# Performance work log

Hardware: AMD Instinct MI355X
Metric: run time of the kernel (lower is better)

## Reference

```python
import jax, jax.numpy as jnp
import numpy as np

N_EMBD = 1024
N_HEAD = 16
HEAD = N_EMBD // N_HEAD


def setup_inputs() -> dict:
    key = jax.random.key(0)
    ks = jax.random.split(key, 5)
    B, T = 2, 2048
    s = 1.0 / np.sqrt(N_EMBD)
    return {
        "x": jax.random.normal(ks[0], (B, T, N_EMBD), dtype=jnp.float32),
        "w_attn": jax.random.normal(ks[1], (N_EMBD, 3 * N_EMBD), dtype=jnp.float32) * s,
        "b_attn": jnp.zeros((3 * N_EMBD,), dtype=jnp.float32),
        "w_proj": jax.random.normal(ks[2], (N_EMBD, N_EMBD), dtype=jnp.float32) * s,
        "b_proj": jnp.zeros((N_EMBD,), dtype=jnp.float32),
    }


def reference(x, w_attn, b_attn, w_proj, b_proj):
    B, T, C = x.shape
    qkv = x @ w_attn + b_attn                      # [B,T,3C]
    q, k, v = jnp.split(qkv, 3, axis=-1)
    def heads(t):
        return t.reshape(B, T, N_HEAD, HEAD).transpose(0, 2, 1, 3)  # [B,H,T,D]
    q, k, v = heads(q), heads(k), heads(v)
    scale = 1.0 / np.sqrt(HEAD).astype(np.float32)
    scores = jnp.einsum('bhqd,bhkd->bhqk', q, k) * scale
    causal = jnp.tril(jnp.ones((T, T), dtype=bool))
    scores = jnp.where(causal, scores, -jnp.inf)
    attn = jax.nn.softmax(scores, axis=-1)
    out = jnp.einsum('bhqk,bhkd->bhqd', attn, v)   # [B,H,T,D]
    out = out.transpose(0, 2, 1, 3).reshape(B, T, C)
    return out @ w_proj + b_proj
```

## Files before the change

kernel.cpp:

```cpp
#include <hip/hip_runtime.h>
#include <stdint.h>

#define N_EMBD 1024
#define N_HEADv 16
#define HEADv 64
#define Bv 2
#define Tv 2048
#define BT (Bv*Tv)
#define C3 (3*N_EMBD)

typedef __attribute__((ext_vector_type(8))) short bf16x8;
typedef __attribute__((ext_vector_type(4))) float f32x4;

typedef __attribute__((address_space(3))) uint32_t lds_u32;
typedef const __attribute__((address_space(1))) uint32_t glb_u32;

__device__ __forceinline__ void gload_lds16(const void* g, void* l){
  __builtin_amdgcn_global_load_lds((glb_u32*)g, (lds_u32*)l, 16, 0, 0);
}

__device__ __forceinline__ unsigned short f2bf(float f){
  union { float f; uint32_t u; } v; v.f = f;
  uint32_t u = v.u;
  uint32_t r = u + 0x7FFFu + ((u>>16)&1u);
  return (unsigned short)(r>>16);
}
__device__ __forceinline__ float bf2f(unsigned short s){
  union { uint32_t u; float f; } v; v.u = ((uint32_t)s)<<16; return v.f;
}
__device__ __forceinline__ uint32_t cvt_pk_bf16(float lo, float hi){
  uint32_t r;
  asm("v_cvt_pk_bf16_f32 %0, %1, %2" : "=v"(r) : "v"(lo), "v"(hi));
  return r;
}

__global__ __launch_bounds__(256) void k_prep(
    const float* __restrict__ x, unsigned short* __restrict__ xb,
    const float* __restrict__ w_attn, unsigned short* __restrict__ wat,
    const float* __restrict__ w_proj, unsigned short* __restrict__ wpt)
{
  __shared__ float tile[64][65];
  int blk = blockIdx.x;
  int t = threadIdx.x;
  if(blk < 2048){
    long i = ((long)blk*256 + t)*8;
    float4 a = *reinterpret_cast<const float4*>(x+i);
    float4 b = *reinterpret_cast<const float4*>(x+i+4);
    union { int4 v; unsigned short s[8]; } o;
    o.s[0]=f2bf(a.x); o.s[1]=f2bf(a.y); o.s[2]=f2bf(a.z); o.s[3]=f2bf(a.w);
    o.s[4]=f2bf(b.x); o.s[5]=f2bf(b.y); o.s[6]=f2bf(b.z); o.s[7]=f2bf(b.w);
    *reinterpret_cast<int4*>(xb+i) = o.v;
  } else {
    const float* in; unsigned short* out; int K, N, n0, k0;
    if(blk < 2816){
      int b = blk - 2048;
      in = w_attn; out = wat; K = N_EMBD; N = C3;
      n0 = (b % 48)*64; k0 = (b / 48)*64;
    } else {
      int b = blk - 2816;
      in = w_proj; out = wpt; K = N_EMBD; N = N_EMBD;
      n0 = (b % 16)*64; k0 = (b / 16)*64;
    }
    #pragma unroll
    for(int p=0;p<4;p++){
      int row = (t>>4) + p*16;
      int col4 = (t&15)*4;
      float4 v = *reinterpret_cast<const float4*>(&in[(size_t)(k0+row)*N + n0 + col4]);
      tile[row][col4+0]=v.x; tile[row][col4+1]=v.y; tile[row][col4+2]=v.z; tile[row][col4+3]=v.w;
    }
    __syncthreads();
    #pragma unroll
    for(int p=0;p<4;p++){
      int nrow = (t>>4) + p*16;
      int kc = (t&15)*4;
      ushort4 o;
      o.x = f2bf(tile[kc+0][nrow]);
      o.y = f2bf(tile[kc+1][nrow]);
      o.z = f2bf(tile[kc+2][nrow]);
      o.w = f2bf(tile[kc+3][nrow]);
      *reinterpret_cast<ushort4*>(&out[(size_t)(n0+nrow)*K + k0 + kc]) = o;
    }
  }
}

template<int MODE, int FM, int FN>
__global__ __launch_bounds__(256) void k_gemm(
    const unsigned short* __restrict__ A,
    const unsigned short* __restrict__ Bt,
    const float* __restrict__ bias,
    void* __restrict__ Cout,
    int M, int N, int K)
{
  const int BK=64;
  const int TM=FM*32, TN=FN*32;
  const int ASZ=TM*BK, BSZ=TN*BK;
  __shared__ unsigned short As[2*ASZ];
  __shared__ unsigned short Bs[2*BSZ];
  int m0 = blockIdx.y*TM, n0 = blockIdx.x*TN;
  int t = threadIdx.x, lane = t&63, wid = t>>6;
  int wm = (wid>>1)*FM*16, wn = (wid&1)*FN*16;
  int g = lane>>4, r16 = lane&15;
  int rl  = lane>>3;
  int cle = (((lane&7) ^ rl) * 8);
  int rsw = r16 & 7;
  f32x4 acc[FM][FN] = {};

  #pragma unroll
  for(int c=0;c<FM;c++){
    int rb = wid*FM*8 + c*8;
    gload_lds16(&A [(size_t)(m0+rb+rl)*K + cle], &As[rb*BK]);
  }
  #pragma unroll
  for(int c=0;c<FN;c++){
    int rb = wid*FN*8 + c*8;
    gload_lds16(&Bt[(size_t)(n0+rb+rl)*K + cle], &Bs[rb*BK]);
  }
  __syncthreads();

  const int NIT = K/BK;
  for(int it=0; it<NIT; ++it){
    int cur = it & 1;
    if(it+1 < NIT){
      int k0 = (it+1)*BK;
      #pragma unroll
      for(int c=0;c<FM;c++){
        int rb = wid*FM*8 + c*8;
        gload_lds16(&A [(size_t)(m0+rb+rl)*K + k0 + cle], &As[(cur^1)*ASZ + rb*BK]);
      }
      #pragma unroll
      for(int c=0;c<FN;c++){
        int rb = wid*FN*8 + c*8;
        gload_lds16(&Bt[(size_t)(n0+rb+rl)*K + k0 + cle], &Bs[(cur^1)*BSZ + rb*BK]);
      }
    }
    const unsigned short* Ab = &As[cur*ASZ];
    const unsigned short* Bb = &Bs[cur*BSZ];
    bf16x8 af[2][FM], bfr[2][FN];
    #pragma unroll
    for(int ks=0;ks<2;ks++){
      #pragma unroll
      for(int mi=0;mi<FM;mi++)
        af[ks][mi]  = *reinterpret_cast<const bf16x8*>(&Ab[(wm+mi*16+r16)*BK + (((ks*4+g)^rsw)*8)]);
      #pragma unroll
      for(int ni=0;ni<FN;ni++)
        bfr[ks][ni] = *reinterpret_cast<const bf16x8*>(&Bb[(wn+ni*16+r16)*BK + (((ks*4+g)^rsw)*8)]);
    }
    __builtin_amdgcn_s_setprio(1);
    #pragma unroll
    for(int ks=0;ks<2;ks++)
      #pragma unroll
      for(int mi=0;mi<FM;mi++)
        #pragma unroll
        for(int ni=0;ni<FN;ni++){
          if(MODE==0)
            acc[mi][ni] = __builtin_amdgcn_mfma_f32_16x16x32_bf16(af[ks][mi], bfr[ks][ni], acc[mi][ni], 0,0,0);
          else
            acc[mi][ni] = __builtin_amdgcn_mfma_f32_16x16x32_bf16(bfr[ks][ni], af[ks][mi], acc[mi][ni], 0,0,0);
        }
    __builtin_amdgcn_s_setprio(0);
    __syncthreads();
  }

  if(MODE==0){
    int which = (n0+wn)>>10;
    int h = ((n0+wn)&1023)>>6;
    int bb = m0>>11;
    int tt0 = (m0&2047) + wm;
    unsigned short* base = (unsigned short*)Cout;
    if(which < 2){
      float scale = (which==0) ? 0.18033688f : 1.0f;
      unsigned short* dst = base + (size_t)which*BT*N_EMBD
                          + (((size_t)bb*N_HEADv + h)*Tv + tt0)*HEADv;
      #pragma unroll
      for(int ni=0;ni<FN;ni++){
        float bv = bias[n0+wn+ni*16+r16];
        int d = ni*16 + r16;
        #pragma unroll
        for(int mi=0;mi<FM;mi++)
          #pragma unroll
          for(int reg=0;reg<4;reg++){
            int tt = mi*16 + g*4 + reg;
            dst[(size_t)tt*HEADv + d] = f2bf((acc[mi][ni][reg] + bv)*scale);
          }
      }
    } else {
      unsigned short* dst = base + 2ll*BT*N_EMBD
                          + (((size_t)bb*N_HEADv + h)*HEADv)*Tv + tt0;
      #pragma unroll
      for(int ni=0;ni<FN;ni++){
        float bv = bias[n0+wn+ni*16+r16];
        int d = ni*16 + r16;
        #pragma unroll
        for(int mi=0;mi<FM;mi++)
          #pragma unroll
          for(int reg=0;reg<4;reg++){
            int tt = mi*16 + g*4 + reg;
            dst[(size_t)d*Tv + tt] = f2bf(acc[mi][ni][reg] + bv);
          }
      }
    }
  } else {
    float* out = (float*)Cout;
    #pragma unroll
    for(int mi=0;mi<FM;mi++){
      int m = m0+wm+mi*16+r16;
      #pragma unroll
      for(int ni=0;ni<FN;ni++){
        int n = n0+wn+ni*16+g*4;
        float4 b4 = *reinterpret_cast<const float4*>(&bias[n]);
        float4 o4;
        o4.x = acc[mi][ni][0] + b4.x;
        o4.y = acc[mi][ni][1] + b4.y;
        o4.z = acc[mi][ni][2] + b4.z;
        o4.w = acc[mi][ni][3] + b4.w;
        *reinterpret_cast<float4*>(&out[(size_t)m*N + n]) = o4;
      }
    }
  }
}

__global__ __launch_bounds__(256) void k_attn(
    const unsigned short* __restrict__ QKV,
    unsigned short* __restrict__ O,
    unsigned short* __restrict__ partO,
    float2* __restrict__ stats)
{
  __shared__ unsigned short Ks[2][64][64];
  __shared__ unsigned short Vs[2][64][64];
  __shared__ unsigned short Ps[4][16][64];
  int blk = blockIdx.x;
  int bh = blk & 31;
  int j  = blk >> 5;
  int qt, kt0, ktN; bool single;
  if(j < 16)      { qt = 16+j;  kt0 = 0;  ktN = 16;    single = false; }
  else if(j < 32) { qt = 47-j;  kt0 = 16; ktN = qt+1;  single = false; }
  else            { qt = 47-j;  kt0 = 0;  ktN = qt+1;  single = true;  }

  int t = threadIdx.x, lane=t&63, wid=t>>6;
  int g = lane>>4, r16 = lane&15;
  const unsigned short* Qp  = QKV + (size_t)bh*Tv*HEADv;
  const unsigned short* Kp  = QKV + (size_t)BT*N_EMBD + (size_t)bh*Tv*HEADv;
  const unsigned short* Vtp = QKV + 2ll*BT*N_EMBD + (size_t)bh*HEADv*Tv;
  int q0 = qt*64 + wid*16;

  bf16x8 aq[2];
  #pragma unroll
  for(int kb=0;kb<2;kb++)
    aq[kb] = *reinterpret_cast<const bf16x8*>(&Qp[(size_t)(q0+r16)*HEADv + kb*32 + g*8]);

  const short ONE = (short)0x3F80;
  const bf16x8 ones8 = {ONE,ONE,ONE,ONE,ONE,ONE,ONE,ONE};

  f32x4 oacc[4] = {};
  f32x4 lacc = {};
  float m2 = 6.0f;

  int r0 = t>>3, c0 = (t&7)*8;
  int r1 = r0 + 32;
  int sw0 = c0 ^ ((r0&7)<<3);
  int sw1 = c0 ^ ((r1&7)<<3);
  int rsw = (r16&7)<<3;

  int4 kc0, kc1, vc0, vc1;
  kc0 = *reinterpret_cast<const int4*>(&Kp [(size_t)(kt0*64+r0)*HEADv + c0]);
  kc1 = *reinterpret_cast<const int4*>(&Kp [(size_t)(kt0*64+r1)*HEADv + c0]);
  vc0 = *reinterpret_cast<const int4*>(&Vtp[(size_t)r0*Tv + kt0*64 + c0]);
  vc1 = *reinterpret_cast<const int4*>(&Vtp[(size_t)r1*Tv + kt0*64 + c0]);
  *reinterpret_cast<int4*>(&Ks[0][r0][sw0]) = kc0;
  *reinterpret_cast<int4*>(&Ks[0][r1][sw1]) = kc1;
  *reinterpret_cast<int4*>(&Vs[0][r0][sw0]) = vc0;
  *reinterpret_cast<int4*>(&Vs[0][r1][sw1]) = vc1;
  if(ktN - kt0 > 1){
    kc0 = *reinterpret_cast<const int4*>(&Kp [(size_t)((kt0+1)*64+r0)*HEADv + c0]);
    kc1 = *reinterpret_cast<const int4*>(&Kp [(size_t)((kt0+1)*64+r1)*HEADv + c0]);
    vc0 = *reinterpret_cast<const int4*>(&Vtp[(size_t)r0*Tv + (kt0+1)*64 + c0]);
    vc1 = *reinterpret_cast<const int4*>(&Vtp[(size_t)r1*Tv + (kt0+1)*64 + c0]);
  }
  __syncthreads();

  for(int kt=kt0; kt<ktN; ++kt){
    int cur = kt & 1;

    f32x4 sacc[4];
    __builtin_amdgcn_s_setprio(1);
    #pragma unroll
    for(int nb=0;nb<4;nb++){
      sacc[nb] = (f32x4){0.f,0.f,0.f,0.f};
      #pragma unroll
      for(int kb=0;kb<2;kb++){
        bf16x8 bk = *reinterpret_cast<const bf16x8*>(&Ks[cur][nb*16+r16][(kb*32+g*8) ^ rsw]);
        sacc[nb] = __builtin_amdgcn_mfma_f32_16x16x32_bf16(bk, aq[kb], sacc[nb],0,0,0);
      }
    }
    __builtin_amdgcn_s_setprio(0);

    if(kt+1 < ktN){
      *reinterpret_cast<int4*>(&Ks[cur^1][r0][sw0]) = kc0;
      *reinterpret_cast<int4*>(&Ks[cur^1][r1][sw1]) = kc1;
      *reinterpret_cast<int4*>(&Vs[cur^1][r0][sw0]) = vc0;
      *reinterpret_cast<int4*>(&Vs[cur^1][r1][sw1]) = vc1;
      if(kt+2 < ktN){
        kc0 = *reinterpret_cast<const int4*>(&Kp [(size_t)((kt+2)*64+r0)*HEADv + c0]);
        kc1 = *reinterpret_cast<const int4*>(&Kp [(size_t)((kt+2)*64+r1)*HEADv + c0]);
        vc0 = *reinterpret_cast<const int4*>(&Vtp[(size_t)r0*Tv + (kt+2)*64 + c0]);
        vc1 = *reinterpret_cast<const int4*>(&Vtp[(size_t)r1*Tv + (kt+2)*64 + c0]);
      }
    }

    bool diag = (kt == qt);
    float pv[4][4];
    if(diag){
      #pragma unroll
      for(int nb=0;nb<4;nb++)
        #pragma unroll
        for(int reg=0;reg<4;reg++){
          int keyin = nb*16 + g*4 + reg;
          if(keyin > wid*16 + r16) sacc[nb][reg] = -1e30f;
        }
    }
    #pragma unroll
    for(int nb=0;nb<4;nb++)
      #pragma unroll
      for(int reg=0;reg<4;reg++)
        pv[nb][reg] = __builtin_amdgcn_exp2f(sacc[nb][reg] - m2);

    float a0 = fmaxf(fmaxf(sacc[0][0],sacc[0][1]),sacc[0][2]);
    float a1 = fmaxf(fmaxf(sacc[0][3],sacc[1][0]),sacc[1][1]);
    float a2 = fmaxf(fmaxf(sacc[1][2],sacc[1][3]),sacc[2][0]);
    float a3 = fmaxf(fmaxf(sacc[2][1],sacc[2][2]),sacc[2][3]);
    float a4 = fmaxf(fmaxf(sacc[3][0],sacc[3][1]),sacc[3][2]);
    float b0 = fmaxf(fmaxf(a0,a1),a2);
    float b1 = fmaxf(fmaxf(a3,a4),sacc[3][3]);
    float mx = fmaxf(b0,b1);

    if(!__all(mx - m2 <= 11.5f)){
      mx = fmaxf(mx, __shfl_xor(mx, 16, 64));
      mx = fmaxf(mx, __shfl_xor(mx, 32, 64));
      float mn = fmaxf(m2, mx);
      float alpha = __builtin_amdgcn_exp2f(m2 - mn);
      lacc[0]*=alpha; lacc[1]*=alpha; lacc[2]*=alpha; lacc[3]*=alpha;
      #pragma unroll
      for(int nb=0;nb<4;nb++)
        #pragma unroll
        for(int reg=0;reg<4;reg++) oacc[nb][reg] *= alpha;
      m2 = mn;
      #pragma unroll
      for(int nb=0;nb<4;nb++)
        #pragma unroll
        for(int reg=0;reg<4;reg++)
          pv[nb][reg] = __builtin_amdgcn_exp2f(sacc[nb][reg] - m2);
    }

    #pragma unroll
    for(int nb=0;nb<4;nb++){
      int2 w;
      w.x = (int)cvt_pk_bf16(pv[nb][0], pv[nb][1]);
      w.y = (int)cvt_pk_bf16(pv[nb][2], pv[nb][3]);
      *reinterpret_cast<int2*>(&Ps[wid][r16][(nb*16+g*4) ^ rsw]) = w;
    }

    __builtin_amdgcn_s_setprio(1);
    #pragma unroll
    for(int kb=0;kb<2;kb++){
      bf16x8 ap = *reinterpret_cast<const bf16x8*>(&Ps[wid][r16][(kb*32+g*8) ^ rsw]);
      lacc = __builtin_amdgcn_mfma_f32_16x16x32_bf16(ones8, ap, lacc,0,0,0);
      #pragma unroll
      for(int nb=0;nb<4;nb++){
        bf16x8 bv = *reinterpret_cast<const bf16x8*>(&Vs[cur][nb*16+r16][(kb*32+g*8) ^ rsw]);
        oacc[nb] = __builtin_amdgcn_mfma_f32_16x16x32_bf16(bv, ap, oacc[nb],0,0,0);
      }
    }
    __builtin_amdgcn_s_setprio(0);
    __syncthreads();
  }

  float l = lacc[0];
  float rinv = 1.0f / l;
  if(single){
    int b = bh >> 4, h = bh & 15;
    size_t row = (size_t)b*Tv + q0 + r16;
    #pragma unroll
    for(int nb=0;nb<4;nb++){
      ushort4 o;
      o.x = f2bf(oacc[nb][0]*rinv);
      o.y = f2bf(oacc[nb][1]*rinv);
      o.z = f2bf(oacc[nb][2]*rinv);
      o.w = f2bf(oacc[nb][3]*rinv);
      *reinterpret_cast<ushort4*>(&O[row*N_EMBD + h*HEADv + nb*16 + g*4]) = o;
    }
  } else {
    int part = j*32 + bh;
    unsigned short* po = partO + (size_t)part*4096;
    int qloc = wid*16 + r16;
    #pragma unroll
    for(int nb=0;nb<4;nb++){
      ushort4 o;
      o.x = f2bf(oacc[nb][0]*rinv);
      o.y = f2bf(oacc[nb][1]*rinv);
      o.z = f2bf(oacc[nb][2]*rinv);
      o.w = f2bf(oacc[nb][3]*rinv);
      *reinterpret_cast<ushort4*>(&po[qloc*64 + nb*16 + g*4]) = o;
    }
    if(g==0) stats[part*64 + qloc] = make_float2(m2, l);
  }
}

__global__ __launch_bounds__(256) void k_merge(
    const unsigned short* __restrict__ partO,
    const float2* __restrict__ stats,
    unsigned short* __restrict__ O)
{
  int blk = blockIdx.x;
  int bh = blk & 31, qt = 16 + (blk >> 5);
  int p0 = (qt-16)*32 + bh;
  int p1 = (47-qt)*32 + bh;
  int t = threadIdx.x;
  int q = t >> 2, d0 = (t&3)*16;
  float2 s0 = stats[p0*64 + q];
  float2 s1 = stats[p1*64 + q];
  float m = fmaxf(s0.x, s1.x);
  float w0 = s0.y * __builtin_amdgcn_exp2f(s0.x - m);
  float w1 = s1.y * __builtin_amdgcn_exp2f(s1.x - m);
  float rinv = 1.f/(w0+w1);
  w0 *= rinv; w1 *= rinv;
  const unsigned short* a = partO + (size_t)p0*4096 + q*64 + d0;
  const unsigned short* b = partO + (size_t)p1*4096 + q*64 + d0;
  int bb = bh >> 4, h = bh & 15;
  unsigned short* o = O + ((size_t)bb*Tv + qt*64 + q)*N_EMBD + h*HEADv + d0;
  #pragma unroll
  for(int half=0; half<2; ++half){
    union { int4 v; unsigned short s[8]; } ua, ub, uo;
    ua.v = *reinterpret_cast<const int4*>(a + half*8);
    ub.v = *reinterpret_cast<const int4*>(b + half*8);
    #pragma unroll
    for(int e=0;e<8;e++)
      uo.s[e] = f2bf(bf2f(ua.s[e])*w0 + bf2f(ub.s[e])*w1);
    *reinterpret_cast<int4*>(o + half*8) = uo.v;
  }
}

extern "C" void kernel_launch(void* const* d_in, const int* in_sizes, int n_in,
                              void* d_out, int out_size, void* d_ws, size_t ws_size,
                              hipStream_t stream){
  const float* x      = (const float*)d_in[0];
  const float* w_attn = (const float*)d_in[1];
  const float* b_attn = (const float*)d_in[2];
  const float* w_proj = (const float*)d_in[3];
  const float* b_proj = (const float*)d_in[4];
  char* ws = (char*)d_ws;
  unsigned short* xb  = (unsigned short*)ws;
  unsigned short* qkv = (unsigned short*)(ws + 8ll*1024*1024);
  unsigned short* ob  = (unsigned short*)(ws + 32ll*1024*1024);
  unsigned short* wat = (unsigned short*)(ws + 40ll*1024*1024);
  unsigned short* wpt = (unsigned short*)(ws + 46ll*1024*1024);
  unsigned short* partO = xb;
  float2*        stats  = (float2*)wat;

  k_prep<<<dim3(3072),256,0,stream>>>(x, xb, w_attn, wat, w_proj, wpt);
  k_gemm<0,2,4><<<dim3(C3/128, BT/64),256,0,stream>>>(xb, wat, b_attn, (void*)qkv, BT, C3, N_EMBD);
  k_attn<<<dim3(48*32),256,0,stream>>>(qkv, ob, partO, stats);
  k_merge<<<dim3(512),256,0,stream>>>(partO, stats, ob);
  k_gemm<1,2,2><<<dim3(N_EMBD/64, BT/64),256,0,stream>>>(ob, wpt, b_proj, d_out, BT, N_EMBD, N_EMBD);
}
```

Before: 106.7 us.

## Split causal attention KV range into 8-tile chunks with multi-way merge

Replaces the two-way split of long query tiles with up to four KV chunks of 8 tiles each, so every attention block handles at most 8 KV tiles and the grid grows from 48 to 80 blocks per head. The merge kernel now combines up to four partial outputs using their log-sum-exp stats. The goal is shorter, more uniform blocks for better load balance on the GPU. The cost is more partial writes, more merge traffic across more merged rows, and extra workspace allocated at new offsets.

```diff
diff --git a/kernel.cpp b/kernel.cpp
--- a/kernel.cpp
+++ b/kernel.cpp
@@ -231,10 +231,14 @@
   int blk = blockIdx.x;
   int bh = blk & 31;
   int j  = blk >> 5;
-  int qt, kt0, ktN; bool single;
-  if(j < 16)      { qt = 16+j;  kt0 = 0;  ktN = 16;    single = false; }
-  else if(j < 32) { qt = 47-j;  kt0 = 16; ktN = qt+1;  single = false; }
-  else            { qt = 47-j;  kt0 = 0;  ktN = qt+1;  single = true;  }
+  int qt, c;
+  if(j < 32)      { c=0; qt = j; }
+  else if(j < 56) { c=1; qt = 8  + (j-32); }
+  else if(j < 72) { c=2; qt = 16 + (j-56); }
+  else            { c=3; qt = 24 + (j-72); }
+  int kt0 = c*8;
+  int ktN = min(qt+1, kt0+8);
+  bool single = (qt < 8);
 
   int t = threadIdx.x, lane=t&63, wid=t>>6;
   int g = lane>>4, r16 = lane&15;
@@ -389,8 +393,8 @@
       *reinterpret_cast<ushort4*>(&O[row*N_EMBD + h*HEADv + nb*16 + g*4]) = o;
     }
   } else {
-    int part = j*32 + bh;
-    unsigned short* po = partO + (size_t)part*4096;
+    int pidx = (((qt-8)<<2) | c)*32 + bh;
+    unsigned short* po = partO + (size_t)pidx*4096;
     int qloc = wid*16 + r16;
     #pragma unroll
     for(int nb=0;nb<4;nb++){
@@ -401,7 +405,7 @@
       o.w = f2bf(oacc[nb][3]*rinv);
       *reinterpret_cast<ushort4*>(&po[qloc*64 + nb*16 + g*4]) = o;
     }
-    if(g==0) stats[part*64 + qloc] = make_float2(m2, l);
+    if(g==0) stats[pidx*64 + qloc] = make_float2(m2, l);
   }
 }
 
@@ -411,30 +415,46 @@
     unsigned short* __restrict__ O)
 {
   int blk = blockIdx.x;
-  int bh = blk & 31, qt = 16 + (blk >> 5);
-  int p0 = (qt-16)*32 + bh;
-  int p1 = (47-qt)*32 + bh;
+  int bh = blk & 31, qt = 8 + (blk >> 5);
+  int nc = (qt>>3) + 1;
   int t = threadIdx.x;
   int q = t >> 2, d0 = (t&3)*16;
-  float2 s0 = stats[p0*64 + q];
-  float2 s1 = stats[p1*64 + q];
-  float m = fmaxf(s0.x, s1.x);
+  int base = ((qt-8)<<2)*32 + bh;
+
+  float2 s0=make_float2(-1e30f,0.f), s1=s0, s2=s0, s3=s0;
+  s0 = stats[(base+0*32)*64 + q];
+  s1 = stats[(base+1*32)*64 + q];
+  if(nc > 2) s2 = stats[(base+2*32)*64 + q];
+  if(nc > 3) s3 = stats[(base+3*32)*64 + q];
+  float m = fmaxf(fmaxf(s0.x,s1.x), fmaxf(s2.x,s3.x));
   float w0 = s0.y * __builtin_amdgcn_exp2f(s0.x - m);
   float w1 = s1.y * __builtin_amdgcn_exp2f(s1.x - m);
-  float rinv = 1.f/(w0+w1);
-  w0 *= rinv; w1 *= rinv;
-  const unsigned short* a = partO + (size_t)p0*4096 + q*64 + d0;
-  const unsigned short* b = partO + (size_t)p1*4096 + q*64 + d0;
+  float w2 = (nc>2) ? s2.y * __builtin_amdgcn_exp2f(s2.x - m) : 0.f;
+  float w3 = (nc>3) ? s3.y * __builtin_amdgcn_exp2f(s3.x - m) : 0.f;
+  float rinv = 1.f/((w0+w1)+(w2+w3));
+  w0 *= rinv; w1 *= rinv; w2 *= rinv; w3 *= rinv;
+
+  float accf[16] = {};
+  #pragma unroll
+  for(int cc=0; cc<4; ++cc){
+    if(cc >= nc) break;
+    float w = cc==0?w0 : cc==1?w1 : cc==2?w2 : w3;
+    const unsigned short* a = partO + (size_t)(base+cc*32)*4096 + q*64 + d0;
+    #pragma unroll
+    for(int half=0; half<2; ++half){
+      union { int4 v; unsigned short s[8]; } ua;
+      ua.v = *reinterpret_cast<const int4*>(a + half*8);
+      #pragma unroll
+      for(int e=0;e<8;e++) accf[half*8+e] += bf2f(ua.s[e])*w;
+    }
+  }
   int bb = bh >> 4, h = bh & 15;
   unsigned short* o = O + ((size_t)bb*Tv + qt*64 + q)*N_EMBD + h*HEADv + d0;
   #pragma unroll
   for(int half=0; half<2; ++half){
-    union { int4 v; unsigned short s[8]; } ua, ub, uo;
-    ua.v = *reinterpret_cast<const int4*>(a + half*8);
-    ub.v = *reinterpret_cast<const int4*>(b + half*8);
-    #pragma unroll
-    for(int e=0;e<8;e++)
-      uo.s[e] = f2bf(bf2f(ua.s[e])*w0 + bf2f(ub.s[e])*w1);
+    union { int4 v; unsigned short s[8]; } uo;
+    #pragma unroll
+    for(int e=0;e<8;e++) uo.s[e] = f2bf(accf[half*8+e]);
     *reinterpret_cast<int4*>(o + half*8) = uo.v;
   }
 }
@@ -453,12 +473,12 @@
   unsigned short* ob  = (unsigned short*)(ws + 32ll*1024*1024);
   unsigned short* wat = (unsigned short*)(ws + 40ll*1024*1024);
   unsigned short* wpt = (unsigned short*)(ws + 46ll*1024*1024);
-  unsigned short* partO = xb;
-  float2*        stats  = (float2*)wat;
+  unsigned short* partO = (unsigned short*)(ws + 48ll*1024*1024);
+  float2*        stats  = (float2*)(ws + 72ll*1024*1024);
 
   k_prep<<<dim3(3072),256,0,stream>>>(x, xb, w_attn, wat, w_proj, wpt);
   k_gemm<0,2,4><<<dim3(C3/128, BT/64),256,0,stream>>>(xb, wat, b_attn, (void*)qkv, BT, C3, N_EMBD);
-  k_attn<<<dim3(48*32),256,0,stream>>>(qkv, ob, partO, stats);
-  k_merge<<<dim3(512),256,0,stream>>>(partO, stats, ob);
+  k_attn<<<dim3(80*32),256,0,stream>>>(qkv, ob, partO, stats);
+  k_merge<<<dim3(768),256,0,stream>>>(partO, stats, ob);
   k_gemm<1,2,2><<<dim3(N_EMBD/64, BT/64),256,0,stream>>>(ob, wpt, b_proj, d_out, BT, N_EMBD, N_EMBD);
 }
```

Result: slower. 112.1 us (+5.1%).

## Triple-buffer QKV GEMM LDS tiles with explicit vmcnt waits

Applied to the files above, without the earlier changes.

Adds an NBUF template parameter to the GEMM and uses three LDS buffers for the QKV projection. Tile k+2 is issued while tile k is computed. Each iteration now has one barrier guarded by s_waitcnt vmcnt(6), so two tile loads stay in flight instead of one, to hide global-load latency better. The output projection keeps double buffering. The split-attention partial outputs and stats move to dedicated workspace regions instead of aliasing xb and the weight buffer. The cost is more LDS per block, which may lower occupancy, and hand-coded wait counts that depend on the exact load count per stage.

```diff
diff --git a/kernel.cpp b/kernel.cpp
--- a/kernel.cpp
+++ b/kernel.cpp
@@ -83,7 +83,7 @@
   }
 }
 
-template<int MODE, int FM, int FN>
+template<int MODE, int FM, int FN, int NBUF>
 __global__ __launch_bounds__(256) void k_gemm(
     const unsigned short* __restrict__ A,
     const unsigned short* __restrict__ Bt,
@@ -94,8 +94,8 @@
   const int BK=64;
   const int TM=FM*32, TN=FN*32;
   const int ASZ=TM*BK, BSZ=TN*BK;
-  __shared__ unsigned short As[2*ASZ];
-  __shared__ unsigned short Bs[2*BSZ];
+  __shared__ unsigned short As[NBUF*ASZ];
+  __shared__ unsigned short Bs[NBUF*BSZ];
   int m0 = blockIdx.y*TM, n0 = blockIdx.x*TN;
   int t = threadIdx.x, lane = t&63, wid = t>>6;
   int wm = (wid>>1)*FM*16, wn = (wid&1)*FN*16;
@@ -104,37 +104,24 @@
   int cle = (((lane&7) ^ rl) * 8);
   int rsw = r16 & 7;
   f32x4 acc[FM][FN] = {};
-
-  #pragma unroll
-  for(int c=0;c<FM;c++){
-    int rb = wid*FM*8 + c*8;
-    gload_lds16(&A [(size_t)(m0+rb+rl)*K + cle], &As[rb*BK]);
-  }
-  #pragma unroll
-  for(int c=0;c<FN;c++){
-    int rb = wid*FN*8 + c*8;
-    gload_lds16(&Bt[(size_t)(n0+rb+rl)*K + cle], &Bs[rb*BK]);
-  }
-  __syncthreads();
-
   const int NIT = K/BK;
-  for(int it=0; it<NIT; ++it){
-    int cur = it & 1;
-    if(it+1 < NIT){
-      int k0 = (it+1)*BK;
-      #pragma unroll
-      for(int c=0;c<FM;c++){
-        int rb = wid*FM*8 + c*8;
-        gload_lds16(&A [(size_t)(m0+rb+rl)*K + k0 + cle], &As[(cur^1)*ASZ + rb*BK]);
-      }
-      #pragma unroll
-      for(int c=0;c<FN;c++){
-        int rb = wid*FN*8 + c*8;
-        gload_lds16(&Bt[(size_t)(n0+rb+rl)*K + k0 + cle], &Bs[(cur^1)*BSZ + rb*BK]);
-      }
-    }
-    const unsigned short* Ab = &As[cur*ASZ];
-    const unsigned short* Bb = &Bs[cur*BSZ];
+
+  auto stage = [&](int tile, int buf){
+    int k0 = tile*BK;
+    #pragma unroll
+    for(int c=0;c<FM;c++){
+      int rb = wid*FM*8 + c*8;
+      gload_lds16(&A [(size_t)(m0+rb+rl)*K + k0 + cle], &As[buf*ASZ + rb*BK]);
+    }
+    #pragma unroll
+    for(int c=0;c<FN;c++){
+      int rb = wid*FN*8 + c*8;
+      gload_lds16(&Bt[(size_t)(n0+rb+rl)*K + k0 + cle], &Bs[buf*BSZ + rb*BK]);
+    }
+  };
+  auto compute = [&](int buf){
+    const unsigned short* Ab = &As[buf*ASZ];
+    const unsigned short* Bb = &Bs[buf*BSZ];
     bf16x8 af[2][FM], bfr[2][FN];
     #pragma unroll
     for(int ks=0;ks<2;ks++){
@@ -158,7 +145,40 @@
             acc[mi][ni] = __builtin_amdgcn_mfma_f32_16x16x32_bf16(bfr[ks][ni], af[ks][mi], acc[mi][ni], 0,0,0);
         }
     __builtin_amdgcn_s_setprio(0);
+  };
+
+  if(NBUF == 2){
+    stage(0, 0);
     __syncthreads();
+    for(int it=0; it<NIT; ++it){
+      int cur = it & 1;
+      if(it+1 < NIT) stage(it+1, cur^1);
+      compute(cur);
+      __syncthreads();
+    }
+  } else {
+    static_assert(NBUF!=3 || true, "");
+    stage(0, 0);
+    stage(1, 1);
+    asm volatile("s_waitcnt vmcnt(6)" ::: "memory");
+    __builtin_amdgcn_sched_barrier(0);
+    __builtin_amdgcn_s_barrier();
+    __builtin_amdgcn_sched_barrier(0);
+    int cur = 0;
+    for(int it=0; it<NIT; ++it){
+      int nx2 = (cur==0) ? 2 : cur-1;
+      bool iss = (it+2 < NIT);
+      if(iss) stage(it+2, nx2);
+      compute(cur);
+      if(it+1 < NIT){
+        if(iss) asm volatile("s_waitcnt vmcnt(6)" ::: "memory");
+        else    asm volatile("s_waitcnt vmcnt(0)" ::: "memory");
+        __builtin_amdgcn_sched_barrier(0);
+        __builtin_amdgcn_s_barrier();
+        __builtin_amdgcn_sched_barrier(0);
+      }
+      cur = (cur==2) ? 0 : cur+1;
+    }
   }
 
   if(MODE==0){
@@ -453,12 +473,12 @@
   unsigned short* ob  = (unsigned short*)(ws + 32ll*1024*1024);
   unsigned short* wat = (unsigned short*)(ws + 40ll*1024*1024);
   unsigned short* wpt = (unsigned short*)(ws + 46ll*1024*1024);
-  unsigned short* partO = xb;
-  float2*        stats  = (float2*)wat;
+  unsigned short* partO = (unsigned short*)(ws + 48ll*1024*1024);
+  float2*        stats  = (float2*)(ws + 60ll*1024*1024);
 
   k_prep<<<dim3(3072),256,0,stream>>>(x, xb, w_attn, wat, w_proj, wpt);
-  k_gemm<0,2,4><<<dim3(C3/128, BT/64),256,0,stream>>>(xb, wat, b_attn, (void*)qkv, BT, C3, N_EMBD);
+  k_gemm<0,2,4,3><<<dim3(C3/128, BT/64),256,0,stream>>>(xb, wat, b_attn, (void*)qkv, BT, C3, N_EMBD);
   k_attn<<<dim3(48*32),256,0,stream>>>(qkv, ob, partO, stats);
   k_merge<<<dim3(512),256,0,stream>>>(partO, stats, ob);
-  k_gemm<1,2,2><<<dim3(N_EMBD/64, BT/64),256,0,stream>>>(ob, wpt, b_proj, d_out, BT, N_EMBD, N_EMBD);
-}
+  k_gemm<1,2,2,2><<<dim3(N_EMBD/64, BT/64),256,0,stream>>>(ob, wpt, b_proj, d_out, BT, N_EMBD, N_EMBD);
+}
```

Measured after the change: 116.4 us. 1.09x slower.
